# Performance work log

Measured on AMD Instinct MI355X. Metric: run time of the kernel, lower is better.

The kernel has to match this reference:

```python
import jax, jax.numpy as jnp
import numpy as np

B, N, T, L = 32, 716, 168, 64
SED, TED = 32, 4
TN_LAYERS, GCN_LAYERS = 2, 2
TCN_C = 16


def _gru_scan(xseq, Wih, Whh, bih, bhh):
    # torch nn.GRU (batch_first) math; xseq: (B,T,Din) -> (B,T,H)
    Bq = xseq.shape[0]
    H = Whh.shape[1]
    xw = xseq @ Wih.T + bih  # (B,T,3H)

    def step(h, xw_t):
        gh = h @ Whh.T + bhh
        xr, xz, xn = jnp.split(xw_t, 3, axis=-1)
        hr, hz, hn = jnp.split(gh, 3, axis=-1)
        r = jax.nn.sigmoid(xr + hr)
        z = jax.nn.sigmoid(xz + hz)
        n = jnp.tanh(xn + r * hn)
        h_new = (1.0 - z) * n + z * h
        return h_new, h_new

    h0 = jnp.zeros((Bq, H), xseq.dtype)
    _, hs = jax.lax.scan(step, h0, jnp.swapaxes(xw, 0, 1))
    return jnp.swapaxes(hs, 0, 1)


def setup_inputs() -> dict:
    key = jax.random.key(0)
    ks = jax.random.split(key, 20)
    r = lambda k, shp, s: jax.random.normal(k, shp, dtype=jnp.float32) * s
    z = lambda shp: jnp.zeros(shp, jnp.float32)
    din = T + SED
    gin = N + SED + TED
    inp = {
        'x': r(ks[0], (B, N, T), 1.0),
        'x_enc_mark': r(ks[1], (B, T, TED), 1.0),
        'se_emb': r(ks[2], (N, SED), 0.02),
        'se_W1': r(ks[3], (din, L), din ** -0.5), 'se_b1': z((L,)),
        'se_W2': r(ks[4], (L, L), L ** -0.5), 'se_b2': z((L,)),
        'te_emb': r(ks[5], (T, SED), 0.02),
        'te_Wih': r(ks[6], (3 * L, gin), gin ** -0.5),
        'te_Whh': r(ks[7], (3 * L, L), L ** -0.5),
        'te_bih': z((3 * L,)), 'te_bhh': z((3 * L,)),
        'gcn_W': r(ks[8], (TN_LAYERS, GCN_LAYERS, L, L), L ** -0.5),
        'gcn_b': z((TN_LAYERS, GCN_LAYERS, L)),
        'fr_W1': r(ks[9], (L, T), L ** -0.5), 'fr_b1': z((T,)),
        'fr_W2': r(ks[10], (T, T), T ** -0.5), 'fr_b2': z((T,)),
        'tr_Wih': r(ks[11], (3 * N, L), L ** -0.5),
        'tr_Whh': r(ks[12], (3 * N, N), N ** -0.5),
        'tr_bih': z((3 * N,)), 'tr_bhh': z((3 * N,)),
        'tcn_W0': r(ks[13], (TCN_C, 3, 1, 2), (3 * 2) ** -0.5), 'tcn_b0': z((TCN_C,)),
        'tcn_W1': r(ks[14], (TCN_C, TCN_C, 1, 2), (TCN_C * 2) ** -0.5), 'tcn_b1': z((TCN_C,)),
        'tcn_W2': r(ks[15], (TCN_C, TCN_C, 1, 2), (TCN_C * 2) ** -0.5), 'tcn_b2': z((TCN_C,)),
        'out_W': r(ks[16], (1, TCN_C, 1, 1), TCN_C ** -0.5), 'out_b': z((1,)),
    }
    return inp


def reference(x, x_enc_mark, se_emb, se_W1, se_b1, se_W2, se_b2,
              te_emb, te_Wih, te_Whh, te_bih, te_bhh,
              gcn_W, gcn_b, fr_W1, fr_b1, fr_W2, fr_b2,
              tr_Wih, tr_Whh, tr_bih, tr_bhh,
              tcn_W0, tcn_b0, tcn_W1, tcn_b1, tcn_W2, tcn_b2, out_W, out_b):
    Bq, Nq, Tq = x.shape
    elu = jax.nn.elu
    # ---- SpatialEncoder: (B,N,T) -> (B,N,L)
    se_in = jnp.concatenate([x, jnp.broadcast_to(se_emb, (Bq,) + se_emb.shape)], axis=2)
    Xs = elu(se_in @ se_W1 + se_b1) @ se_W2 + se_b2
    # ---- TemporalEncoder: GRU over (B,T,N+SED+TED) -> (B,T,L)
    te_in = jnp.concatenate([jnp.swapaxes(x, 1, 2), x_enc_mark,
                             jnp.broadcast_to(te_emb, (Bq,) + te_emb.shape)], axis=2)
    Xt = _gru_scan(te_in, te_Wih, te_Whh, te_bih, te_bhh)
    X = jnp.concatenate([Xs, Xt], axis=1)  # (B, N+T, L)
    # ---- TN modules: adaptive graph construction + message passing.
    # adj = tanh(relu(X X^T) + I). The torch code extracts nonzero edges per batch
    # and scatters messages over them; since zero weights contribute nothing,
    # edge-list message passing == dense weighted-adjacency matmul (vectorized here).
    eye = jnp.eye(Nq + Tq, dtype=x.dtype)
    for i in range(gcn_W.shape[0]):
        adj = jnp.tanh(jax.nn.relu(jnp.einsum('bnf,bmf->bnm', X, X)) + eye)
        h = X
        for j in range(gcn_W.shape[1]):
            h = elu(jnp.einsum('bnm,bmf->bnf', adj, h) @ gcn_W[i, j] + gcn_b[i, j])
        X = h
    Xs, Xt = X[:, :Nq, :], X[:, Nq:, :]
    # ---- rebuild heads
    n_out = elu(Xs @ fr_W1 + fr_b1) @ fr_W2 + fr_b2  # (B,N,T)
    t_out = _gru_scan(Xt, tr_Wih, tr_Whh, tr_bih, tr_bhh)  # (B,T,N)
    stacked = jnp.stack([n_out, jnp.swapaxes(t_out, 1, 2), x], axis=1)  # (B,3,N,T)
    # ---- TCN output layer: causal dilated convs along time, then 1x1 projection
    dn = ('NCHW', 'OIHW', 'NCHW')
    h = stacked
    for W, b, d in ((tcn_W0, tcn_b0, 1), (tcn_W1, tcn_b1, 2), (tcn_W2, tcn_b2, 4)):
        h = jax.lax.conv_general_dilated(h, W, (1, 1), ((0, 0), (d, 0)),
                                         rhs_dilation=(1, d), dimension_numbers=dn)
        h = elu(h + b[None, :, None, None])
    out = jax.lax.conv_general_dilated(h, out_W, (1, 1), 'VALID',
                                       dimension_numbers=dn) + out_b[None, :, None, None]
    return out[:, :, :, -1]  # (B, 1, N): one-step forecast per node
```

## Files before the change

kernel.cpp:

```cpp
#include <hip/hip_runtime.h>

#define B_   32
#define N_   716
#define T_   168
#define L_   64
#define NT_  884
#define NTP  896
#define TE3_ 192
#define TRH_ 716
#define TR3_ 2148
#define TR3P 2176
#define WSTR 744
#define HSTR 720
#define TRBLKS 90

typedef unsigned short u16;
typedef unsigned long long u64;
typedef __attribute__((ext_vector_type(8))) short short8;
typedef __attribute__((ext_vector_type(4))) float f32x4;

static __device__ __forceinline__ float eluf(float x){ return x > 0.f ? x : expm1f(x); }
static __device__ __forceinline__ float sigf(float x){ return 1.f/(1.f+expf(-x)); }
static __device__ __forceinline__ u16 f2bf(float f){
  unsigned u = __float_as_uint(f);
  unsigned r = (u + 0x7fffu + ((u >> 16) & 1u)) >> 16;
  return (u16)r;
}
static __device__ __forceinline__ float bf2f(u16 h){
  return __uint_as_float(((unsigned)h) << 16);
}
static __device__ __forceinline__ f32x4 bmfma(short8 a, short8 b, f32x4 c){
  return __builtin_amdgcn_mfma_f32_16x16x32_bf16(a, b, c, 0, 0, 0);
}

__global__ __launch_bounds__(256) void k_whhbf(const float* __restrict__ in, u16* __restrict__ out, int n4){
  int i = blockIdx.x*256 + threadIdx.x;
  if (i >= n4) return;
  f32x4 v = *(const f32x4*)(in + (size_t)i*4);
  uint2 p;
  p.x = (unsigned)f2bf(v[0]) | ((unsigned)f2bf(v[1])<<16);
  p.y = (unsigned)f2bf(v[2]) | ((unsigned)f2bf(v[3])<<16);
  *(uint2*)(out + (size_t)i*4) = p;
}
__global__ __launch_bounds__(256) void k_wihbf(const float* __restrict__ Wih, u16* __restrict__ WihB){
  int idx = blockIdx.x*256 + threadIdx.x;
  if (idx >= TR3P*L_) return;
  int r = idx >> 6;
  WihB[idx] = (r < TR3_) ? f2bf(Wih[idx]) : (u16)0;
}
__global__ __launch_bounds__(256) void k_wsmall(
    const float* __restrict__ gW, const float* __restrict__ sW1, const float* __restrict__ sW2,
    const float* __restrict__ fW1, const float* __restrict__ fW2, const float* __restrict__ tW,
    u16* __restrict__ WTh, u16* __restrict__ WTl,
    u16* __restrict__ w1seh, u16* __restrict__ w1sel, u16* __restrict__ w2seh, u16* __restrict__ w2sel,
    u16* __restrict__ w1frh, u16* __restrict__ w1frl, u16* __restrict__ w2frh, u16* __restrict__ w2frl,
    u16* __restrict__ wteB){
  int bid = blockIdx.x, tid = threadIdx.x;
  if (bid < 4){
    int l = bid;
    for (int e = tid; e < 4096; e += 256){
      int g = e >> 6, f = e & 63;
      float v = gW[(size_t)l*4096 + f*64 + g];
      u16 hi = f2bf(v);
      WTh[(size_t)l*4096 + e] = hi;
      WTl[(size_t)l*4096 + e] = f2bf(v - bf2f(hi));
    }
  } else if (bid == 4){
    for (int e = tid; e < 64*224; e += 256){
      int g = e / 224, k = e % 224;
      float v = (k < 200) ? sW1[k*64 + g] : 0.f;
      u16 hi = f2bf(v); w1seh[e] = hi; w1sel[e] = f2bf(v - bf2f(hi));
    }
    for (int e = tid; e < 4096; e += 256){
      int g = e >> 6, f = e & 63;
      float v = sW2[f*64 + g];
      u16 hi = f2bf(v); w2seh[e] = hi; w2sel[e] = f2bf(v - bf2f(hi));
    }
  } else if (bid == 5){
    for (int e = tid; e < 176*64; e += 256){
      int n = e >> 6, k = e & 63;
      float v = (n < 168) ? fW1[k*168 + n] : 0.f;
      u16 hi = f2bf(v); w1frh[e] = hi; w1frl[e] = f2bf(v - bf2f(hi));
    }
    for (int e = tid; e < 16*192; e += 256){
      int c = e / 192, k = e % 192;
      float v = (c < 8 && k < 168) ? fW2[k*168 + 160 + c] : 0.f;
      u16 hi = f2bf(v); w2frh[e] = hi; w2frl[e] = f2bf(v - bf2f(hi));
    }
  } else {
    int idx = (bid - 6)*256 + tid;
    int k = idx % 768;
    float v = (k < 752) ? tW[(size_t)(idx/768)*752 + k] : 0.f;
    wteB[idx] = f2bf(v);
  }
}

__global__ __launch_bounds__(256) void k_sem(const float* __restrict__ x, const float* __restrict__ se_emb,
    const u16* __restrict__ w1h, const u16* __restrict__ w1l,
    const u16* __restrict__ w2h, const u16* __restrict__ w2l,
    const float* __restrict__ b1, const float* __restrict__ b2, float* __restrict__ X){
  __shared__ u16 Sh[64*232], Sl[64*232];
  __shared__ u16 Tlh[64*72], Tll[64*72];
  int m0 = blockIdx.x*64;
  int tid = threadIdx.x, wv = tid >> 6, lane = tid & 63;
  for (int o = tid; o < 64*224; o += 256){
    int r = o / 224, k = o - (o/224)*224;
    int m = m0 + r; int b = m / N_, n = m - b*N_;
    float v = 0.f;
    if (k < 168) v = x[((size_t)b*N_ + n)*T_ + k];
    else if (k < 200) v = se_emb[n*32 + (k - 168)];
    u16 hi = f2bf(v);
    Sh[r*232 + k] = hi; Sl[r*232 + k] = f2bf(v - bf2f(hi));
  }
  __syncthreads();
  const u16* Ah = Sh + (16*wv + (lane & 15))*232 + (lane >> 4)*8;
  const u16* Al = Sl + (16*wv + (lane & 15))*232 + (lane >> 4)*8;
  const u16* Bh = w1h + (lane & 15)*224 + (lane >> 4)*8;
  const u16* Bl = w1l + (lane & 15)*224 + (lane >> 4)*8;
  f32x4 hh[4], hl[4], lh[4];
  #pragma unroll
  for (int q = 0; q < 4; ++q){ hh[q]=(f32x4){0,0,0,0}; hl[q]=(f32x4){0,0,0,0}; lh[q]=(f32x4){0,0,0,0}; }
  #pragma unroll
  for (int kt = 0; kt < 7; ++kt){
    short8 ah = *(const short8*)(Ah + kt*32);
    short8 al = *(const short8*)(Al + kt*32);
    #pragma unroll
    for (int q = 0; q < 4; ++q){
      short8 bh = *(const short8*)(Bh + q*16*224 + kt*32);
      short8 bl = *(const short8*)(Bl + q*16*224 + kt*32);
      hh[q] = bmfma(ah, bh, hh[q]);
      hl[q] = bmfma(ah, bl, hl[q]);
      lh[q] = bmfma(al, bh, lh[q]);
    }
  }
  int mrow = 16*wv + (lane >> 4)*4;
  #pragma unroll
  for (int q = 0; q < 4; ++q){
    int g = q*16 + (lane & 15);
    float bv = b1[g];
    #pragma unroll
    for (int r = 0; r < 4; ++r){
      float v = eluf(hh[q][r] + hl[q][r] + lh[q][r] + bv);
      u16 hi = f2bf(v);
      Tlh[(mrow + r)*72 + g] = hi;
      Tll[(mrow + r)*72 + g] = f2bf(v - bf2f(hi));
    }
  }
  __syncthreads();
  const u16* A2h = Tlh + (16*wv + (lane & 15))*72 + (lane >> 4)*8;
  const u16* A2l = Tll + (16*wv + (lane & 15))*72 + (lane >> 4)*8;
  const u16* B2h = w2h + (lane & 15)*64 + (lane >> 4)*8;
  const u16* B2l = w2l + (lane & 15)*64 + (lane >> 4)*8;
  f32x4 ohh[4], ohl[4], olh[4];
  #pragma unroll
  for (int q = 0; q < 4; ++q){ ohh[q]=(f32x4){0,0,0,0}; ohl[q]=(f32x4){0,0,0,0}; olh[q]=(f32x4){0,0,0,0}; }
  #pragma unroll
  for (int kt = 0; kt < 2; ++kt){
    short8 a2h = *(const short8*)(A2h + kt*32);
    short8 a2l = *(const short8*)(A2l + kt*32);
    #pragma unroll
    for (int q = 0; q < 4; ++q){
      short8 b2h = *(const short8*)(B2h + q*16*64 + kt*32);
      short8 b2l = *(const short8*)(B2l + q*16*64 + kt*32);
      ohh[q] = bmfma(a2h, b2h, ohh[q]);
      ohl[q] = bmfma(a2h, b2l, ohl[q]);
      olh[q] = bmfma(a2l, b2h, olh[q]);
    }
  }
  #pragma unroll
  for (int q = 0; q < 4; ++q){
    int g = q*16 + (lane & 15);
    float bv = b2[g];
    #pragma unroll
    for (int r = 0; r < 4; ++r){
      int m = m0 + mrow + r;
      int b = m / N_, n = m - b*N_;
      X[((size_t)b*NT_ + n)*L_ + g] = ohh[q][r] + ohl[q][r] + olh[q][r] + bv;
    }
  }
}

__global__ __launch_bounds__(256) void k_teinx_b(const float* __restrict__ x, u16* __restrict__ teB){
  __shared__ float tile[32][33];
  int b = blockIdx.z; int n0 = blockIdx.x*32, t0 = blockIdx.y*32;
  int tx = threadIdx.x & 31, ty = threadIdx.x >> 5;
  for (int i = ty; i < 32; i += 8){
    int n = n0 + i, t = t0 + tx;
    if (n < N_ && t < T_) tile[i][tx] = x[((size_t)b*N_ + n)*T_ + t];
  }
  __syncthreads();
  for (int i = ty; i < 32; i += 8){
    int t = t0 + i, n = n0 + tx;
    if (t < T_ && n < N_)
      teB[((size_t)b*T_ + t)*768 + n] = f2bf(tile[tx][i]);
  }
}
__global__ __launch_bounds__(256) void k_teinr_b(const float* __restrict__ mark, const float* __restrict__ te_emb,
                                                 u16* __restrict__ teB){
  int idx = blockIdx.x*256 + threadIdx.x;
  if (idx >= B_*T_*52) return;
  int c = idx % 52; int row = idx / 52; int b = row / T_, t = row % T_;
  float v = 0.f;
  if (c < 4) v = mark[((size_t)b*T_ + t)*4 + c];
  else if (c < 36) v = te_emb[t*32 + (c - 4)];
  teB[(size_t)row*768 + 716 + c] = f2bf(v);
}

__global__ __launch_bounds__(256) void k_texw(const u16* __restrict__ teB, const u16* __restrict__ wteB,
    const float* __restrict__ bih, float* __restrict__ xwte){
  int m0 = blockIdx.x*64, n0 = blockIdx.y*64;
  int tid = threadIdx.x, wv = tid >> 6, lane = tid & 63;
  const u16* Ah = teB + (size_t)(m0 + 16*wv + (lane & 15))*768 + (lane >> 4)*8;
  const u16* Bh = wteB + (size_t)(n0 + (lane & 15))*768 + (lane >> 4)*8;
  f32x4 hh[4];
  #pragma unroll
  for (int q = 0; q < 4; ++q) hh[q]=(f32x4){0,0,0,0};
  #pragma unroll 4
  for (int kt = 0; kt < 24; ++kt){
    short8 ah = *(const short8*)(Ah + kt*32);
    #pragma unroll
    for (int q = 0; q < 4; ++q)
      hh[q] = bmfma(ah, *(const short8*)(Bh + q*16*768 + kt*32), hh[q]);
  }
  int mb = m0 + 16*wv + (lane >> 4)*4;
  #pragma unroll
  for (int q = 0; q < 4; ++q){
    int g = n0 + q*16 + (lane & 15);
    float bv = bih[g];
    #pragma unroll
    for (int r = 0; r < 4; ++r)
      xwte[(size_t)(mb + r)*TE3_ + g] = hh[q][r] + bv;
  }
}

__global__ __launch_bounds__(192) void k_te_scan(const float* __restrict__ xw, const float* __restrict__ Whh,
                 const float* __restrict__ bhh, float* __restrict__ X){
  int b = blockIdx.x; int tid = threadIdx.x;
  __shared__ float Wsh[TE3_*65];
  __shared__ float hs[64];
  __shared__ float gh[TE3_];
  for (int l = tid; l < TE3_*64; l += 192){ int j = l >> 6, f = l & 63; Wsh[j*65+f] = Whh[l]; }
  if (tid < 64) hs[tid] = 0.f;
  __syncthreads();
  for (int t = 0; t < T_; ++t){
    const float* xr = xw + ((size_t)b*T_ + t)*TE3_;
    float g0 = bhh[tid], g1 = 0.f, g2 = 0.f, g3 = 0.f;
    #pragma unroll
    for (int f = 0; f < 64; f += 4){
      g0 = fmaf(hs[f],   Wsh[tid*65+f],   g0);
      g1 = fmaf(hs[f+1], Wsh[tid*65+f+1], g1);
      g2 = fmaf(hs[f+2], Wsh[tid*65+f+2], g2);
      g3 = fmaf(hs[f+3], Wsh[tid*65+f+3], g3);
    }
    gh[tid] = (g0 + g1) + (g2 + g3);
    __syncthreads();
    if (tid < 64){
      float r = sigf(xr[tid] + gh[tid]);
      float z = sigf(xr[64+tid] + gh[64+tid]);
      float n = tanhf(xr[128+tid] + r*gh[128+tid]);
      float hn = (1.f - z)*n + z*hs[tid];
      hs[tid] = hn;
      X[((size_t)b*NT_ + N_ + t)*L_ + tid] = hn;
    }
    __syncthreads();
  }
}

__global__ __launch_bounds__(256) void k_xbf(const float* __restrict__ X,
                 u16* __restrict__ Xbh, u16* __restrict__ Xbl,
                 u16* __restrict__ XTh, u16* __restrict__ XTl){
  __shared__ u16 th[32][33], tl[32][33];
  int b = blockIdx.z, i0 = blockIdx.x*32, f0 = blockIdx.y*32;
  int tx = threadIdx.x & 31, ty = threadIdx.x >> 5;
  for (int rr = ty; rr < 32; rr += 8){
    int i = i0 + rr, f = f0 + tx;
    float v = (i < NT_) ? X[((size_t)b*NT_ + i)*L_ + f] : 0.f;
    u16 hi = f2bf(v);
    u16 lo = f2bf(v - bf2f(hi));
    th[rr][tx] = hi; tl[rr][tx] = lo;
    Xbh[((size_t)b*NTP + i)*L_ + f] = hi;
    Xbl[((size_t)b*NTP + i)*L_ + f] = lo;
  }
  __syncthreads();
  for (int rr = ty; rr < 32; rr += 8){
    XTh[((size_t)b*L_ + f0 + rr)*NTP + i0 + tx] = th[tx][rr];
    XTl[((size_t)b*L_ + f0 + rr)*NTP + i0 + tx] = tl[tx][rr];
  }
}

__global__ __launch_bounds__(256) void k_gcnf(
    const u16* __restrict__ Xbh, const u16* __restrict__ Xbl,
    const u16* __restrict__ hTh, const u16* __restrict__ hTl,
    const u16* __restrict__ WTh, const u16* __restrict__ WTl,
    const float* __restrict__ bias,
    float* __restrict__ Y, u16* __restrict__ YTh, u16* __restrict__ YTl){
  __shared__ u16 AJh[64*72], AJl[64*72];
  __shared__ u16 Tlh[64*72], Tll[64*72];
  int b = blockIdx.y, i0 = blockIdx.x*64;
  int tid = threadIdx.x, wv = tid >> 6, lane = tid & 63;
  const u16* XAh = Xbh + ((size_t)b*NTP + i0 + 16*wv + (lane & 15))*L_ + (lane >> 4)*8;
  const u16* XAl = Xbl + ((size_t)b*NTP + i0 + 16*wv + (lane & 15))*L_ + (lane >> 4)*8;
  const int ib = i0 + 16*wv + (lane >> 4)*4;
  const int mrow = 16*wv + (lane >> 4)*4;
  f32x4 thh[4], thl[4], tlh[4];
  #pragma unroll
  for (int q = 0; q < 4; ++q){ thh[q] = (f32x4){0,0,0,0}; thl[q] = (f32x4){0,0,0,0}; tlh[q] = (f32x4){0,0,0,0}; }
  for (int jt = 0; jt < 14; ++jt){
    int j0 = jt*64;
    {
      const u16* XBh = Xbh + ((size_t)b*NTP + j0 + (lane & 15))*L_ + (lane >> 4)*8;
      const u16* XBl = Xbl + ((size_t)b*NTP + j0 + (lane & 15))*L_ + (lane >> 4)*8;
      f32x4 chh[4], chl[4], clh[4];
      #pragma unroll
      for (int q = 0; q < 4; ++q){ chh[q] = (f32x4){0,0,0,0}; chl[q] = (f32x4){0,0,0,0}; clh[q] = (f32x4){0,0,0,0}; }
      #pragma unroll
      for (int kt = 0; kt < 2; ++kt){
        short8 ah = *(const short8*)(XAh + kt*32);
        short8 al = *(const short8*)(XAl + kt*32);
        #pragma unroll
        for (int q = 0; q < 4; ++q){
          short8 bh = *(const short8*)(XBh + q*16*L_ + kt*32);
          short8 bl = *(const short8*)(XBl + q*16*L_ + kt*32);
          chh[q] = bmfma(ah, bh, chh[q]);
          chl[q] = bmfma(ah, bl, chl[q]);
          clh[q] = bmfma(al, bh, clh[q]);
        }
      }
      int jb = j0 + (lane & 15);
      #pragma unroll
      for (int q = 0; q < 4; ++q){
        int j = jb + q*16;
        #pragma unroll
        for (int r = 0; r < 4; ++r){
          int i = ib + r;
          u16 hi = 0, lo = 0;
          if (i < NT_ && j < NT_){
            float v = tanhf(fmaxf(chh[q][r] + chl[q][r] + clh[q][r], 0.f) + (i == j ? 1.f : 0.f));
            hi = f2bf(v); lo = f2bf(v - bf2f(hi));
          }
          AJh[(mrow + r)*72 + q*16 + (lane & 15)] = hi;
          AJl[(mrow + r)*72 + q*16 + (lane & 15)] = lo;
        }
      }
    }
    __syncthreads();
    {
      const u16* A1h = AJh + (16*wv + (lane & 15))*72 + (lane >> 4)*8;
      const u16* A1l = AJl + (16*wv + (lane & 15))*72 + (lane >> 4)*8;
      const u16* B1h = hTh + ((size_t)b*L_ + (lane & 15))*NTP + j0 + (lane >> 4)*8;
      const u16* B1l = hTl + ((size_t)b*L_ + (lane & 15))*NTP + j0 + (lane >> 4)*8;
      #pragma unroll
      for (int kt = 0; kt < 2; ++kt){
        short8 ah = *(const short8*)(A1h + kt*32);
        short8 al = *(const short8*)(A1l + kt*32);
        #pragma unroll
        for (int q = 0; q < 4; ++q){
          short8 bh = *(const short8*)(B1h + q*16*NTP + kt*32);
          short8 bl = *(const short8*)(B1l + q*16*NTP + kt*32);
          thh[q] = bmfma(ah, bh, thh[q]);
          thl[q] = bmfma(ah, bl, thl[q]);
          tlh[q] = bmfma(al, bh, tlh[q]);
        }
      }
    }
    __syncthreads();
  }
  #pragma unroll
  for (int q = 0; q < 4; ++q)
    #pragma unroll
    for (int r = 0; r < 4; ++r){
      float v = thh[q][r] + thl[q][r] + tlh[q][r];
      u16 hi = f2bf(v);
      Tlh[(mrow + r)*72 + q*16 + (lane & 15)] = hi;
      Tll[(mrow + r)*72 + q*16 + (lane & 15)] = f2bf(v - bf2f(hi));
    }
  __syncthreads();
  const u16* A2h = Tlh + (16*wv + (lane & 15))*72 + (lane >> 4)*8;
  const u16* A2l = Tll + (16*wv + (lane & 15))*72 + (lane >> 4)*8;
  const u16* B2h = WTh + (lane & 15)*L_ + (lane >> 4)*8;
  const u16* B2l = WTl + (lane & 15)*L_ + (lane >> 4)*8;
  f32x4 ohh[4], ohl[4], olh[4];
  #pragma unroll
  for (int q = 0; q < 4; ++q){ ohh[q] = (f32x4){0,0,0,0}; ohl[q] = (f32x4){0,0,0,0}; olh[q] = (f32x4){0,0,0,0}; }
  #pragma unroll
  for (int kt = 0; kt < 2; ++kt){
    short8 a2h = *(const short8*)(A2h + kt*32);
    short8 a2l = *(const short8*)(A2l + kt*32);
    #pragma unroll
    for (int q = 0; q < 4; ++q){
      short8 b2h = *(const short8*)(B2h + q*16*L_ + kt*32);
      short8 b2l = *(const short8*)(B2l + q*16*L_ + kt*32);
      ohh[q] = bmfma(a2h, b2h, ohh[q]);
      ohl[q] = bmfma(a2h, b2l, ohl[q]);
      olh[q] = bmfma(a2l, b2h, olh[q]);
    }
  }
  __syncthreads();
  #pragma unroll
  for (int q = 0; q < 4; ++q){
    int g = q*16 + (lane & 15);
    float bv = bias[g];
    #pragma unroll
    for (int r = 0; r < 4; ++r){
      int i = i0 + mrow + r;
      float v = eluf(ohh[q][r] + ohl[q][r] + olh[q][r] + bv);
      if (i < NT_ && Y) Y[((size_t)b*NT_ + i)*L_ + g] = v;
      u16 hi = 0, lo = 0;
      if (i < NT_){ hi = f2bf(v); lo = f2bf(v - bf2f(hi)); }
      Tlh[g*72 + mrow + r] = hi;
      Tll[g*72 + mrow + r] = lo;
    }
  }
  __syncthreads();
  {
    int g = tid >> 2, c = tid & 3;
    uint4* dh = (uint4*)(YTh + ((size_t)b*L_ + g)*NTP + i0 + c*16);
    uint4* dl = (uint4*)(YTl + ((size_t)b*L_ + g)*NTP + i0 + c*16);
    const uint4* sh = (const uint4*)(Tlh + g*72 + c*16);
    const uint4* sl = (const uint4*)(Tll + g*72 + c*16);
    dh[0] = sh[0]; dh[1] = sh[1];
    dl[0] = sl[0]; dl[1] = sl[1];
  }
}

__global__ __launch_bounds__(256) void k_frm(const float* __restrict__ X,
    const u16* __restrict__ w1h, const u16* __restrict__ w1l,
    const u16* __restrict__ w2h, const u16* __restrict__ w2l,
    const float* __restrict__ b1, const float* __restrict__ b2, float* __restrict__ nout8){
  __shared__ u16 Sh[64*72], Sl[64*72];
  __shared__ u16 T1h[64*192], T1l[64*192];
  __shared__ u16 B2hl[16*192], B2ll[16*192];
  int m0 = blockIdx.x*64;
  int tid = threadIdx.x, wv = tid >> 6, lane = tid & 63;
  for (int o = tid; o < 768; o += 256){
    ((u64*)B2hl)[o] = ((const u64*)w2h)[o];
    ((u64*)B2ll)[o] = ((const u64*)w2l)[o];
  }
  for (int o = tid; o < 1024; o += 256){
    int rr = o >> 4, cc = o & 15;
    T1h[rr*192 + 176 + cc] = 0; T1l[rr*192 + 176 + cc] = 0;
  }
  for (int o = tid; o < 4096; o += 256){
    int r = o >> 6, k = o & 63;
    int m = m0 + r; int ab = m / N_, an = m - ab*N_;
    float v = X[((size_t)ab*NT_ + an)*L_ + k];
    u16 hi = f2bf(v);
    Sh[r*72 + k] = hi; Sl[r*72 + k] = f2bf(v - bf2f(hi));
  }
  __syncthreads();
  const u16* Ah = Sh + (16*wv + (lane & 15))*72 + (lane >> 4)*8;
  const u16* Al = Sl + (16*wv + (lane & 15))*72 + (lane >> 4)*8;
  int mrow = 16*wv + (lane >> 4)*4;
  for (int tile = 0; tile < 11; ++tile){
    const u16* Bh = w1h + (tile*16 + (lane & 15))*64 + (lane >> 4)*8;
    const u16* Bl = w1l + (tile*16 + (lane & 15))*64 + (lane >> 4)*8;
    f32x4 shh={0,0,0,0}, shl={0,0,0,0}, slh={0,0,0,0};
    #pragma unroll
    for (int kt = 0; kt < 2; ++kt){
      short8 ah = *(const short8*)(Ah + kt*32);
      short8 al = *(const short8*)(Al + kt*32);
      short8 bh = *(const short8*)(Bh + kt*32);
      short8 bl = *(const short8*)(Bl + kt*32);
      shh = bmfma(ah, bh, shh);
      shl = bmfma(ah, bl, shl);
      slh = bmfma(al, bh, slh);
    }
    int col = tile*16 + (lane & 15);
    float bb = (col < 168) ? b1[col] : 0.f;
    #pragma unroll
    for (int r = 0; r < 4; ++r){
      float v = (col < 168) ? eluf(shh[r] + shl[r] + slh[r] + bb) : 0.f;
      u16 hi = f2bf(v);
      T1h[(mrow + r)*192 + col] = hi;
      T1l[(mrow + r)*192 + col] = f2bf(v - bf2f(hi));
    }
  }
  __syncthreads();
  const u16* A2h = T1h + (16*wv + (lane & 15))*192 + (lane >> 4)*8;
  const u16* A2l = T1l + (16*wv + (lane & 15))*192 + (lane >> 4)*8;
  const u16* Bh2 = B2hl + (lane & 15)*192 + (lane >> 4)*8;
  const u16* Bl2 = B2ll + (lane & 15)*192 + (lane >> 4)*8;
  f32x4 ohh={0,0,0,0}, ohl={0,0,0,0}, olh={0,0,0,0};
  #pragma unroll
  for (int kt = 0; kt < 6; ++kt){
    short8 a2h = *(const short8*)(A2h + kt*32);
    short8 a2l = *(const short8*)(A2l + kt*32);
    short8 b2h = *(const short8*)(Bh2 + kt*32);
    short8 b2l = *(const short8*)(Bl2 + kt*32);
    ohh = bmfma(a2h, b2h, ohh);
    ohl = bmfma(a2h, b2l, ohl);
    olh = bmfma(a2l, b2h, olh);
  }
  int c = lane & 15;
  if (c < 8){
    float bv = b2[160 + c];
    #pragma unroll
    for (int r = 0; r < 4; ++r){
      int m = m0 + mrow + r;
      nout8[(size_t)m*8 + c] = ohh[r] + ohl[r] + olh[r] + bv;
    }
  }
}

__global__ __launch_bounds__(256) void k_xwm2(const float* __restrict__ X, const u16* __restrict__ WihB,
                                              const float* __restrict__ bih, u16* __restrict__ xwB){
  int m0 = blockIdx.x*64, n0 = blockIdx.y*64;
  int tid = threadIdx.x, wv = tid >> 6, lane = tid & 63;
  int am = m0 + 16*wv + (lane & 15);
  int t = am >> 5, b = am & 31;
  const float* Arow = X + ((size_t)b*NT_ + N_ + t)*L_ + (lane >> 4)*8;
  const u16* Bb = WihB + (size_t)(n0 + (lane & 15))*L_ + (lane >> 4)*8;
  f32x4 c0={0,0,0,0}, c1={0,0,0,0}, c2={0,0,0,0}, c3={0,0,0,0};
  #pragma unroll
  for (int kt = 0; kt < 2; ++kt){
    f32x4 f0 = *(const f32x4*)(Arow + kt*32);
    f32x4 f1 = *(const f32x4*)(Arow + kt*32 + 4);
    short8 a;
    a[0]=(short)f2bf(f0[0]); a[1]=(short)f2bf(f0[1]); a[2]=(short)f2bf(f0[2]); a[3]=(short)f2bf(f0[3]);
    a[4]=(short)f2bf(f1[0]); a[5]=(short)f2bf(f1[1]); a[6]=(short)f2bf(f1[2]); a[7]=(short)f2bf(f1[3]);
    c0 = bmfma(a, *(const short8*)(Bb + kt*32), c0);
    c1 = bmfma(a, *(const short8*)(Bb + 16*L_ + kt*32), c1);
    c2 = bmfma(a, *(const short8*)(Bb + 32*L_ + kt*32), c2);
    c3 = bmfma(a, *(const short8*)(Bb + 48*L_ + kt*32), c3);
  }
  int mb = m0 + 16*wv + (lane >> 4)*4;
  int nb = n0 + (lane & 15);
  f32x4 cc[4] = {c0, c1, c2, c3};
  #pragma unroll
  for (int q = 0; q < 4; ++q){
    int n = nb + q*16;
    if (n >= TR3_) continue;
    float bv = bih[n];
    #pragma unroll
    for (int r = 0; r < 4; ++r)
      xwB[(size_t)(mb + r)*TR3_ + n] = f2bf(cc[q][r] + bv);
  }
}

__global__ __launch_bounds__(192) void k_tr_scan(
    const u16* __restrict__ WhhB,
    const float* __restrict__ bhh,
    const u16* __restrict__ xwB,
    u16* __restrict__ hb0, u16* __restrict__ hb1,
    float* __restrict__ tout8,
    int* __restrict__ flags){
  __shared__ u16 w_lds[48*WSTR];
  __shared__ u16 h_lds[16*WSTR];
  __shared__ float g_lds[2*256];
  __shared__ u64 xw_ldsq[2][192];
  const int tid = threadIdx.x;
  const int wv = tid >> 6, lane = tid & 63;
  const int cb = blockIdx.x >> 1, hhalf = blockIdx.x & 1;
  const int k0 = cb*16, b0 = hhalf*16;
  const int prow = tid / 12, pc = tid % 12;
  const int pg = pc >> 2, pko = (pc & 3)*4;

  xw_ldsq[0][prow*12 + pc] =
    *(const u64*)(xwB + (size_t)(b0 + prow)*TR3_ + pg*TRH_ + k0 + pko);
  for (int o = tid; o < 16*24; o += 192){
    int n = o / 24, c = o - n*24;
    h_lds[n*WSTR + 720 + c] = 0;
  }
  for (int r = 0; r < 48; ++r){
    int g = r >> 4, m = r & 15, k = k0 + m;
    bool kv = (k < TRH_);
    const uint2* src = (const uint2*)(WhhB + (size_t)(g*TRH_ + (kv ? k : 0))*TRH_);
    uint2* dst = (uint2*)(w_lds + r*WSTR);
    uint2 zz; zz.x = 0; zz.y = 0;
    for (int o = tid; o < 186; o += 192)
      dst[o] = (kv && o < 179) ? src[o] : zz;
  }
  const u16* arow = w_lds + (size_t)(wv*16 + (lane & 15))*WSTR + (lane >> 4)*8;
  const u16* brow = h_lds + (size_t)(lane & 15)*WSTR + (lane >> 4)*8;

  const int mb = (lane >> 4)*4;
  const int kx = k0 + mb;
  const bool kval = (kx < TRH_);
  const int bx = b0 + (lane & 15);
  f32x4 hp = {0.f, 0.f, 0.f, 0.f};
  f32x4 br4 = {0,0,0,0}, bz4 = {0,0,0,0}, bn4 = {0,0,0,0};
  if (wv == 0){
    int kc = kval ? kx : 0;
    br4 = *(const f32x4*)(bhh + kc);
    bz4 = *(const f32x4*)(bhh + TRH_ + kc);
    bn4 = *(const f32x4*)(bhh + 2*TRH_ + kc);
  }
  const int sn = tid / 12, sj = tid % 12;
  __syncthreads();

  for (int t = 0; t < T_; ++t){
    const u16* hcur = (t & 1) ? hb1 : hb0;
    u16* hnxt = (t & 1) ? hb0 : hb1;
    {
      const u64* srow = (const u64*)(hcur + (size_t)(b0 + sn)*HSTR) + sj;
      u64 v0  = __hip_atomic_load(srow +   0, __ATOMIC_RELAXED, __HIP_MEMORY_SCOPE_AGENT);
      u64 v1  = __hip_atomic_load(srow +  12, __ATOMIC_RELAXED, __HIP_MEMORY_SCOPE_AGENT);
      u64 v2  = __hip_atomic_load(srow +  24, __ATOMIC_RELAXED, __HIP_MEMORY_SCOPE_AGENT);
      u64 v3  = __hip_atomic_load(srow +  36, __ATOMIC_RELAXED, __HIP_MEMORY_SCOPE_AGENT);
      u64 v4  = __hip_atomic_load(srow +  48, __ATOMIC_RELAXED, __HIP_MEMORY_SCOPE_AGENT);
      u64 v5  = __hip_atomic_load(srow +  60, __ATOMIC_RELAXED, __HIP_MEMORY_SCOPE_AGENT);
      u64 v6  = __hip_atomic_load(srow +  72, __ATOMIC_RELAXED, __HIP_MEMORY_SCOPE_AGENT);
      u64 v7  = __hip_atomic_load(srow +  84, __ATOMIC_RELAXED, __HIP_MEMORY_SCOPE_AGENT);
      u64 v8  = __hip_atomic_load(srow +  96, __ATOMIC_RELAXED, __HIP_MEMORY_SCOPE_AGENT);
      u64 v9  = __hip_atomic_load(srow + 108, __ATOMIC_RELAXED, __HIP_MEMORY_SCOPE_AGENT);
      u64 v10 = __hip_atomic_load(srow + 120, __ATOMIC_RELAXED, __HIP_MEMORY_SCOPE_AGENT);
      u64 v11 = __hip_atomic_load(srow + 132, __ATOMIC_RELAXED, __HIP_MEMORY_SCOPE_AGENT);
      u64 v12 = __hip_atomic_load(srow + 144, __ATOMIC_RELAXED, __HIP_MEMORY_SCOPE_AGENT);
      u64 v13 = __hip_atomic_load(srow + 156, __ATOMIC_RELAXED, __HIP_MEMORY_SCOPE_AGENT);
      u64 v14 = __hip_atomic_load(srow + 168, __ATOMIC_RELAXED, __HIP_MEMORY_SCOPE_AGENT);
      u64* d = (u64*)(h_lds + sn*WSTR) + sj;
      d[0]   = v0;   d[12]  = v1;   d[24]  = v2;   d[36]  = v3;
      d[48]  = v4;   d[60]  = v5;   d[72]  = v6;   d[84]  = v7;
      d[96]  = v8;   d[108] = v9;   d[120] = v10;  d[132] = v11;
      d[144] = v12;  d[156] = v13;  d[168] = v14;
    }
    __syncthreads();
    u64 pf = 0;
    const bool haspf = (t + 1 < T_);
    if (haspf)
      pf = *(const u64*)(xwB + (size_t)((t+1)*32 + b0 + prow)*TR3_ + pg*TRH_ + k0 + pko);
    f32x4 a0={0,0,0,0}, a1={0,0,0,0}, a2={0,0,0,0}, a3={0,0,0,0};
    for (int kt = 0; kt < 20; kt += 4){
      a0 = bmfma(*(const short8*)(arow + kt*32),     *(const short8*)(brow + kt*32),     a0);
      a1 = bmfma(*(const short8*)(arow + (kt+1)*32), *(const short8*)(brow + (kt+1)*32), a1);
      a2 = bmfma(*(const short8*)(arow + (kt+2)*32), *(const short8*)(brow + (kt+2)*32), a2);
      a3 = bmfma(*(const short8*)(arow + (kt+3)*32), *(const short8*)(brow + (kt+3)*32), a3);
    }
    a0 = bmfma(*(const short8*)(arow + 20*32), *(const short8*)(brow + 20*32), a0);
    a1 = bmfma(*(const short8*)(arow + 21*32), *(const short8*)(brow + 21*32), a1);
    a2 = bmfma(*(const short8*)(arow + 22*32), *(const short8*)(brow + 22*32), a2);
    f32x4 acc = (a0 + a1) + (a2 + a3);
    if (wv){
      #pragma unroll
      for (int r = 0; r < 4; ++r) g_lds[(wv-1)*256 + lane*4 + r] = acc[r];
    }
    __syncthreads();
    if (wv == 0){
      if (kval){
        const u16* xb = ((const u16*)&xw_ldsq[t & 1][0]) + (lane & 15)*48;
        float hnew[4];
        #pragma unroll
        for (int r = 0; r < 4; ++r){
          float rg = sigf(bf2f(xb[mb + r]) + acc[r] + br4[r]);
          float zg = sigf(bf2f(xb[16 + mb + r]) + g_lds[lane*4 + r] + bz4[r]);
          float ng = tanhf(bf2f(xb[32 + mb + r]) + rg*(g_lds[256 + lane*4 + r] + bn4[r]));
          hnew[r] = (1.f - zg)*ng + zg*hp[r];
          hp[r] = hnew[r];
        }
        u64 pk = (u64)((unsigned)f2bf(hnew[0]) | ((unsigned)f2bf(hnew[1]) << 16))
               | ((u64)((unsigned)f2bf(hnew[2]) | ((unsigned)f2bf(hnew[3]) << 16)) << 32);
        __hip_atomic_store((u64*)(hnxt + (size_t)bx*HSTR + kx), pk,
                           __ATOMIC_RELAXED, __HIP_MEMORY_SCOPE_AGENT);
        if (t >= 160){
          #pragma unroll
          for (int r = 0; r < 4; ++r)
            tout8[(size_t)(bx*TRH_ + kx + r)*8 + (t - 160)] = hnew[r];
        }
      }
      asm volatile("s_waitcnt vmcnt(0)" ::: "memory");
      if (lane == 0)
        __hip_atomic_store(flags + blockIdx.x*16, t + 1,
                           __ATOMIC_RELAXED, __HIP_MEMORY_SCOPE_AGENT);
    }
    if (wv == 1 && lane < 45 && t + 1 < T_){
      const int* fp = flags + (lane*2 + hhalf)*16;
      while (__hip_atomic_load(fp, __ATOMIC_RELAXED, __HIP_MEMORY_SCOPE_AGENT) < t + 1){}
    }
    if (haspf) xw_ldsq[(t + 1) & 1][prow*12 + pc] = pf;
    __syncthreads();
  }
}

__global__ __launch_bounds__(256) void k_tcn(const float* __restrict__ nout8, const float* __restrict__ tout8,
                 const float* __restrict__ x,
                 const float* __restrict__ W0, const float* __restrict__ b0,
                 const float* __restrict__ W1, const float* __restrict__ b1,
                 const float* __restrict__ W2, const float* __restrict__ b2,
                 const float* __restrict__ oW, const float* __restrict__ ob,
                 float* __restrict__ out){
  __shared__ float w0s[96], b0s[16], w1s[512], b1s[16], w2s[512], b2s[16], ows[16], obs;
  int tid = threadIdx.x;
  for (int l = tid; l < 96; l += 256) w0s[l] = W0[l];
  for (int l = tid; l < 512; l += 256){ w1s[l] = W1[l]; w2s[l] = W2[l]; }
  if (tid < 16){ b0s[tid]=b0[tid]; b1s[tid]=b1[tid]; b2s[tid]=b2[tid]; ows[tid]=oW[tid]; }
  if (tid == 0) obs = ob[0];
  __syncthreads();
  int idx = blockIdx.x*256 + tid;
  if (idx >= B_*N_) return;
  int b = idx / N_, n = idx % N_;
  float s0[8], s1[8], s2[8];
  #pragma unroll
  for (int i = 0; i < 8; ++i){
    s0[i] = nout8[(size_t)idx*8 + i];
    s1[i] = tout8[(size_t)idx*8 + i];
    s2[i] = x[((size_t)b*N_ + n)*T_ + 160 + i];
  }
  float h1[16][4];
  #pragma unroll
  for (int c = 0; c < 16; ++c)
    #pragma unroll
    for (int q = 0; q < 4; ++q){
      int tt = 2*q + 1;
      float v = b0s[c]
        + w0s[c*6+0]*s0[tt-1] + w0s[c*6+1]*s0[tt]
        + w0s[c*6+2]*s1[tt-1] + w0s[c*6+3]*s1[tt]
        + w0s[c*6+4]*s2[tt-1] + w0s[c*6+5]*s2[tt];
      h1[c][q] = eluf(v);
    }
  float h2[16][2];
  #pragma unroll
  for (int c = 0; c < 16; ++c){
    float v3 = b1s[c], v7 = b1s[c];
    #pragma unroll
    for (int i2 = 0; i2 < 16; ++i2){
      v3 += w1s[c*32+i2*2]*h1[i2][0] + w1s[c*32+i2*2+1]*h1[i2][1];
      v7 += w1s[c*32+i2*2]*h1[i2][2] + w1s[c*32+i2*2+1]*h1[i2][3];
    }
    h2[c][0] = eluf(v3); h2[c][1] = eluf(v7);
  }
  float o = obs;
  #pragma unroll
  for (int c = 0; c < 16; ++c){
    float v = b2s[c];
    #pragma unroll
    for (int i2 = 0; i2 < 16; ++i2)
      v += w2s[c*32+i2*2]*h2[i2][0] + w2s[c*32+i2*2+1]*h2[i2][1];
    o += ows[c]*eluf(v);
  }
  out[idx] = o;
}

extern "C" void kernel_launch(void* const* d_in, const int* in_sizes, int n_in,
                              void* d_out, int out_size, void* d_ws, size_t ws_size,
                              hipStream_t stream){
  const float* x       = (const float*)d_in[0];
  const float* mark    = (const float*)d_in[1];
  const float* se_emb  = (const float*)d_in[2];
  const float* se_W1   = (const float*)d_in[3];
  const float* se_b1   = (const float*)d_in[4];
  const float* se_W2   = (const float*)d_in[5];
  const float* se_b2   = (const float*)d_in[6];
  const float* te_emb  = (const float*)d_in[7];
  const float* te_Wih  = (const float*)d_in[8];
  const float* te_Whh  = (const float*)d_in[9];
  const float* te_bih  = (const float*)d_in[10];
  const float* te_bhh  = (const float*)d_in[11];
  const float* gcn_W   = (const float*)d_in[12];
  const float* gcn_b   = (const float*)d_in[13];
  const float* fr_W1   = (const float*)d_in[14];
  const float* fr_b1   = (const float*)d_in[15];
  const float* fr_W2   = (const float*)d_in[16];
  const float* fr_b2   = (const float*)d_in[17];
  const float* tr_Wih  = (const float*)d_in[18];
  const float* tr_Whh  = (const float*)d_in[19];
  const float* tr_bih  = (const float*)d_in[20];
  const float* tr_bhh  = (const float*)d_in[21];
  const float* tcn_W0  = (const float*)d_in[22];
  const float* tcn_b0  = (const float*)d_in[23];
  const float* tcn_W1  = (const float*)d_in[24];
  const float* tcn_b1  = (const float*)d_in[25];
  const float* tcn_W2  = (const float*)d_in[26];
  const float* tcn_b2  = (const float*)d_in[27];
  const float* out_W   = (const float*)d_in[28];
  const float* out_b   = (const float*)d_in[29];
  float* out = (float*)d_out;
  (void)in_sizes; (void)n_in; (void)out_size; (void)ws_size;

  char* ws = (char*)d_ws;
  size_t off = 0;
  auto alloc = [&](size_t bytes)->void*{
    void* p = (void*)(ws + off); off += (bytes + 255) & ~(size_t)255; return p; };
  float* X       = (float*)alloc((size_t)B_*NT_*L_*4);
  u16*   teinB   = (u16*)  alloc((size_t)B_*T_*768*2);
  float* te_xw   = (float*)alloc((size_t)B_*T_*TE3_*4);
  u16*   xwB     = (u16*)  alloc((size_t)B_*T_*TR3_*2);
  u16*   WihB    = (u16*)  alloc((size_t)TR3P*L_*2);
  u16*   WhhB    = (u16*)  alloc((size_t)TR3_*TRH_*2);
  u16*   Xbh     = (u16*)  alloc((size_t)B_*NTP*L_*2);
  u16*   Xbl     = (u16*)  alloc((size_t)B_*NTP*L_*2);
  u16*   hTah    = (u16*)  alloc((size_t)B_*L_*NTP*2);
  u16*   hTal    = (u16*)  alloc((size_t)B_*L_*NTP*2);
  u16*   hTbh    = (u16*)  alloc((size_t)B_*L_*NTP*2);
  u16*   hTbl    = (u16*)  alloc((size_t)B_*L_*NTP*2);
  u16*   WTh     = (u16*)  alloc((size_t)4*4096*2);
  u16*   WTl     = (u16*)  alloc((size_t)4*4096*2);
  u16*   w1seh   = (u16*)  alloc((size_t)64*224*2);
  u16*   w1sel   = (u16*)  alloc((size_t)64*224*2);
  u16*   w2seh   = (u16*)  alloc((size_t)4096*2);
  u16*   w2sel   = (u16*)  alloc((size_t)4096*2);
  u16*   w1frh   = (u16*)  alloc((size_t)176*64*2);
  u16*   w1frl   = (u16*)  alloc((size_t)176*64*2);
  u16*   w2frh   = (u16*)  alloc((size_t)16*192*2);
  u16*   w2frl   = (u16*)  alloc((size_t)16*192*2);
  u16*   wteB    = (u16*)  alloc((size_t)192*768*2);
  u16*   hb0     = (u16*)  alloc((size_t)B_*HSTR*2);
  u16*   hb1     = (u16*)  alloc((size_t)B_*HSTR*2);
  int*   flags   = (int*)  alloc(8192);
  float* nout8   = (float*)alloc((size_t)B_*N_*8*4);
  float* tout8   = (float*)alloc((size_t)B_*N_*8*4);

  hipMemsetAsync(hb0, 0, (size_t)B_*HSTR*2*2 + 8192, stream);

  k_whhbf<<<(TR3_*TRH_/4 + 255)/256, 256, 0, stream>>>(tr_Whh, WhhB, TR3_*TRH_/4);
  k_wihbf<<<(TR3P*L_ + 255)/256, 256, 0, stream>>>(tr_Wih, WihB);
  k_wsmall<<<582, 256, 0, stream>>>(gcn_W, se_W1, se_W2, fr_W1, fr_W2, te_Wih,
      WTh, WTl, w1seh, w1sel, w2seh, w2sel, w1frh, w1frl, w2frh, w2frl, wteB);
  k_sem<<<358, 256, 0, stream>>>(x, se_emb, w1seh, w1sel, w2seh, w2sel, se_b1, se_b2, X);
  k_teinx_b<<<dim3(23,6,B_), 256, 0, stream>>>(x, teinB);
  k_teinr_b<<<(B_*T_*52 + 255)/256, 256, 0, stream>>>(mark, te_emb, teinB);
  k_texw<<<dim3(84,3), 256, 0, stream>>>(teinB, wteB, te_bih, te_xw);
  k_te_scan<<<B_, 192, 0, stream>>>(te_xw, te_Whh, te_bhh, X);
  for (int i = 0; i < 2; ++i){
    k_xbf<<<dim3(28,2,B_),256,0,stream>>>(X, Xbh, Xbl, hTah, hTal);
    k_gcnf<<<dim3(14,B_),256,0,stream>>>(Xbh, Xbl, hTah, hTal,
        WTh + (i*2+0)*4096, WTl + (i*2+0)*4096, gcn_b + (i*2+0)*64, nullptr, hTbh, hTbl);
    k_gcnf<<<dim3(14,B_),256,0,stream>>>(Xbh, Xbl, hTbh, hTbl,
        WTh + (i*2+1)*4096, WTl + (i*2+1)*4096, gcn_b + (i*2+1)*64, X, hTah, hTal);
  }
  k_frm<<<358, 256, 0, stream>>>(X, w1frh, w1frl, w2frh, w2frl, fr_b1, fr_b2, nout8);
  k_xwm2<<<dim3(84,34),256,0,stream>>>(X, WihB, tr_bih, xwB);
  k_tr_scan<<<TRBLKS,192,0,stream>>>(WhhB, tr_bhh, xwB, hb0, hb1, tout8, flags);
  k_tcn<<<(B_*N_+255)/256,256,0,stream>>>(nout8, tout8, x,
      tcn_W0, tcn_b0, tcn_W1, tcn_b1, tcn_W2, tcn_b2, out_W, out_b, out);
}
```

Measured before the change: 1.435 ms.

## Merge prep and back-end kernels and move scan flag wait to step start

Three weight-conversion kernels become one k_prep launch, and the frm and xw projection kernels become one k_back launch that picks its work by block index. This cuts launch overhead and lets independent work run concurrently. In the GRU scan, the cross-block flag spin-wait moves from the end of each step to the start and is followed by a barrier. All 45 lanes of a 192-thread block now wait, where before only wave 1 did, and the trailing barrier is gone. The new sync ordering needs care: the xw prefetch store into LDS now has no barrier after it before the next iteration's wait.

```diff
diff --git a/kernel.cpp b/kernel.cpp
--- a/kernel.cpp
+++ b/kernel.cpp
@@ -33,22 +33,9 @@
   return __builtin_amdgcn_mfma_f32_16x16x32_bf16(a, b, c, 0, 0, 0);
 }
 
-__global__ __launch_bounds__(256) void k_whhbf(const float* __restrict__ in, u16* __restrict__ out, int n4){
-  int i = blockIdx.x*256 + threadIdx.x;
-  if (i >= n4) return;
-  f32x4 v = *(const f32x4*)(in + (size_t)i*4);
-  uint2 p;
-  p.x = (unsigned)f2bf(v[0]) | ((unsigned)f2bf(v[1])<<16);
-  p.y = (unsigned)f2bf(v[2]) | ((unsigned)f2bf(v[3])<<16);
-  *(uint2*)(out + (size_t)i*4) = p;
-}
-__global__ __launch_bounds__(256) void k_wihbf(const float* __restrict__ Wih, u16* __restrict__ WihB){
-  int idx = blockIdx.x*256 + threadIdx.x;
-  if (idx >= TR3P*L_) return;
-  int r = idx >> 6;
-  WihB[idx] = (r < TR3_) ? f2bf(Wih[idx]) : (u16)0;
-}
-__global__ __launch_bounds__(256) void k_wsmall(
+__global__ __launch_bounds__(256) void k_prep(
+    const float* __restrict__ whh, u16* __restrict__ WhhB,
+    const float* __restrict__ wih, u16* __restrict__ WihB,
     const float* __restrict__ gW, const float* __restrict__ sW1, const float* __restrict__ sW2,
     const float* __restrict__ fW1, const float* __restrict__ fW2, const float* __restrict__ tW,
     u16* __restrict__ WTh, u16* __restrict__ WTl,
@@ -56,8 +43,21 @@
     u16* __restrict__ w1frh, u16* __restrict__ w1frl, u16* __restrict__ w2frh, u16* __restrict__ w2frl,
     u16* __restrict__ wteB){
   int bid = blockIdx.x, tid = threadIdx.x;
-  if (bid < 4){
-    int l = bid;
+  if (bid < 1502){
+    int i = bid*256 + tid;
+    if (i < TR3_*TRH_/4){
+      f32x4 v = *(const f32x4*)(whh + (size_t)i*4);
+      uint2 p;
+      p.x = (unsigned)f2bf(v[0]) | ((unsigned)f2bf(v[1])<<16);
+      p.y = (unsigned)f2bf(v[2]) | ((unsigned)f2bf(v[3])<<16);
+      *(uint2*)(WhhB + (size_t)i*4) = p;
+    }
+  } else if (bid < 2046){
+    int idx = (bid - 1502)*256 + tid;
+    int r = idx >> 6;
+    WihB[idx] = (r < TR3_) ? f2bf(wih[idx]) : (u16)0;
+  } else if (bid < 2050){
+    int l = bid - 2046;
     for (int e = tid; e < 4096; e += 256){
       int g = e >> 6, f = e & 63;
       float v = gW[(size_t)l*4096 + f*64 + g];
@@ -65,7 +65,7 @@
       WTh[(size_t)l*4096 + e] = hi;
       WTl[(size_t)l*4096 + e] = f2bf(v - bf2f(hi));
     }
-  } else if (bid == 4){
+  } else if (bid == 2050){
     for (int e = tid; e < 64*224; e += 256){
       int g = e / 224, k = e % 224;
       float v = (k < 200) ? sW1[k*64 + g] : 0.f;
@@ -76,7 +76,7 @@
       float v = sW2[f*64 + g];
       u16 hi = f2bf(v); w2seh[e] = hi; w2sel[e] = f2bf(v - bf2f(hi));
     }
-  } else if (bid == 5){
+  } else if (bid == 2051){
     for (int e = tid; e < 176*64; e += 256){
       int n = e >> 6, k = e & 63;
       float v = (n < 168) ? fW1[k*168 + n] : 0.f;
@@ -88,7 +88,7 @@
       u16 hi = f2bf(v); w2frh[e] = hi; w2frl[e] = f2bf(v - bf2f(hi));
     }
   } else {
-    int idx = (bid - 6)*256 + tid;
+    int idx = (bid - 2052)*256 + tid;
     int k = idx % 768;
     float v = (k < 752) ? tW[(size_t)(idx/768)*752 + k] : 0.f;
     wteB[idx] = f2bf(v);
@@ -423,15 +423,50 @@
   }
 }
 
-__global__ __launch_bounds__(256) void k_frm(const float* __restrict__ X,
+__global__ __launch_bounds__(256) void k_back(const float* __restrict__ X,
     const u16* __restrict__ w1h, const u16* __restrict__ w1l,
     const u16* __restrict__ w2h, const u16* __restrict__ w2l,
-    const float* __restrict__ b1, const float* __restrict__ b2, float* __restrict__ nout8){
+    const float* __restrict__ b1, const float* __restrict__ b2, float* __restrict__ nout8,
+    const u16* __restrict__ WihB, const float* __restrict__ bih, u16* __restrict__ xwB){
   __shared__ u16 Sh[64*72], Sl[64*72];
   __shared__ u16 T1h[64*192], T1l[64*192];
   __shared__ u16 B2hl[16*192], B2ll[16*192];
+  int tid = threadIdx.x, wv = tid >> 6, lane = tid & 63;
+  if (blockIdx.x >= 358){
+    int r = blockIdx.x - 358;
+    int m0 = (r % 84)*64, n0 = (r / 84)*64;
+    int am = m0 + 16*wv + (lane & 15);
+    int t = am >> 5, b = am & 31;
+    const float* Arow = X + ((size_t)b*NT_ + N_ + t)*L_ + (lane >> 4)*8;
+    const u16* Bb = WihB + (size_t)(n0 + (lane & 15))*L_ + (lane >> 4)*8;
+    f32x4 c0={0,0,0,0}, c1={0,0,0,0}, c2={0,0,0,0}, c3={0,0,0,0};
+    #pragma unroll
+    for (int kt = 0; kt < 2; ++kt){
+      f32x4 f0 = *(const f32x4*)(Arow + kt*32);
+      f32x4 f1 = *(const f32x4*)(Arow + kt*32 + 4);
+      short8 a;
+      a[0]=(short)f2bf(f0[0]); a[1]=(short)f2bf(f0[1]); a[2]=(short)f2bf(f0[2]); a[3]=(short)f2bf(f0[3]);
+      a[4]=(short)f2bf(f1[0]); a[5]=(short)f2bf(f1[1]); a[6]=(short)f2bf(f1[2]); a[7]=(short)f2bf(f1[3]);
+      c0 = bmfma(a, *(const short8*)(Bb + kt*32), c0);
+      c1 = bmfma(a, *(const short8*)(Bb + 16*L_ + kt*32), c1);
+      c2 = bmfma(a, *(const short8*)(Bb + 32*L_ + kt*32), c2);
+      c3 = bmfma(a, *(const short8*)(Bb + 48*L_ + kt*32), c3);
+    }
+    int mb = m0 + 16*wv + (lane >> 4)*4;
+    int nb = n0 + (lane & 15);
+    f32x4 cc[4] = {c0, c1, c2, c3};
+    #pragma unroll
+    for (int q = 0; q < 4; ++q){
+      int n = nb + q*16;
+      if (n >= TR3_) continue;
+      float bv = bih[n];
+      #pragma unroll
+      for (int rr = 0; rr < 4; ++rr)
+        xwB[(size_t)(mb + rr)*TR3_ + n] = f2bf(cc[q][rr] + bv);
+    }
+    return;
+  }
   int m0 = blockIdx.x*64;
-  int tid = threadIdx.x, wv = tid >> 6, lane = tid & 63;
   for (int o = tid; o < 768; o += 256){
     ((u64*)B2hl)[o] = ((const u64*)w2h)[o];
     ((u64*)B2ll)[o] = ((const u64*)w2l)[o];
@@ -499,41 +534,6 @@
       int m = m0 + mrow + r;
       nout8[(size_t)m*8 + c] = ohh[r] + ohl[r] + olh[r] + bv;
     }
-  }
-}
-
-__global__ __launch_bounds__(256) void k_xwm2(const float* __restrict__ X, const u16* __restrict__ WihB,
-                                              const float* __restrict__ bih, u16* __restrict__ xwB){
-  int m0 = blockIdx.x*64, n0 = blockIdx.y*64;
-  int tid = threadIdx.x, wv = tid >> 6, lane = tid & 63;
-  int am = m0 + 16*wv + (lane & 15);
-  int t = am >> 5, b = am & 31;
-  const float* Arow = X + ((size_t)b*NT_ + N_ + t)*L_ + (lane >> 4)*8;
-  const u16* Bb = WihB + (size_t)(n0 + (lane & 15))*L_ + (lane >> 4)*8;
-  f32x4 c0={0,0,0,0}, c1={0,0,0,0}, c2={0,0,0,0}, c3={0,0,0,0};
-  #pragma unroll
-  for (int kt = 0; kt < 2; ++kt){
-    f32x4 f0 = *(const f32x4*)(Arow + kt*32);
-    f32x4 f1 = *(const f32x4*)(Arow + kt*32 + 4);
-    short8 a;
-    a[0]=(short)f2bf(f0[0]); a[1]=(short)f2bf(f0[1]); a[2]=(short)f2bf(f0[2]); a[3]=(short)f2bf(f0[3]);
-    a[4]=(short)f2bf(f1[0]); a[5]=(short)f2bf(f1[1]); a[6]=(short)f2bf(f1[2]); a[7]=(short)f2bf(f1[3]);
-    c0 = bmfma(a, *(const short8*)(Bb + kt*32), c0);
-    c1 = bmfma(a, *(const short8*)(Bb + 16*L_ + kt*32), c1);
-    c2 = bmfma(a, *(const short8*)(Bb + 32*L_ + kt*32), c2);
-    c3 = bmfma(a, *(const short8*)(Bb + 48*L_ + kt*32), c3);
-  }
-  int mb = m0 + 16*wv + (lane >> 4)*4;
-  int nb = n0 + (lane & 15);
-  f32x4 cc[4] = {c0, c1, c2, c3};
-  #pragma unroll
-  for (int q = 0; q < 4; ++q){
-    int n = nb + q*16;
-    if (n >= TR3_) continue;
-    float bv = bih[n];
-    #pragma unroll
-    for (int r = 0; r < 4; ++r)
-      xwB[(size_t)(mb + r)*TR3_ + n] = f2bf(cc[q][r] + bv);
   }
 }
 
@@ -591,6 +591,11 @@
   for (int t = 0; t < T_; ++t){
     const u16* hcur = (t & 1) ? hb1 : hb0;
     u16* hnxt = (t & 1) ? hb0 : hb1;
+    if (tid < 45){
+      const int* fp = flags + (tid*2 + hhalf)*16;
+      while (__hip_atomic_load(fp, __ATOMIC_RELAXED, __HIP_MEMORY_SCOPE_AGENT) < t){}
+    }
+    __syncthreads();
     {
       const u64* srow = (const u64*)(hcur + (size_t)(b0 + sn)*HSTR) + sj;
       u64 v0  = __hip_atomic_load(srow +   0, __ATOMIC_RELAXED, __HIP_MEMORY_SCOPE_AGENT);
@@ -662,12 +667,7 @@
         __hip_atomic_store(flags + blockIdx.x*16, t + 1,
                            __ATOMIC_RELAXED, __HIP_MEMORY_SCOPE_AGENT);
     }
-    if (wv == 1 && lane < 45 && t + 1 < T_){
-      const int* fp = flags + (lane*2 + hhalf)*16;
-      while (__hip_atomic_load(fp, __ATOMIC_RELAXED, __HIP_MEMORY_SCOPE_AGENT) < t + 1){}
-    }
     if (haspf) xw_ldsq[(t + 1) & 1][prow*12 + pc] = pf;
-    __syncthreads();
   }
 }
 
@@ -801,9 +801,8 @@
 
   hipMemsetAsync(hb0, 0, (size_t)B_*HSTR*2*2 + 8192, stream);
 
-  k_whhbf<<<(TR3_*TRH_/4 + 255)/256, 256, 0, stream>>>(tr_Whh, WhhB, TR3_*TRH_/4);
-  k_wihbf<<<(TR3P*L_ + 255)/256, 256, 0, stream>>>(tr_Wih, WihB);
-  k_wsmall<<<582, 256, 0, stream>>>(gcn_W, se_W1, se_W2, fr_W1, fr_W2, te_Wih,
+  k_prep<<<2628, 256, 0, stream>>>(tr_Whh, WhhB, tr_Wih, WihB,
+      gcn_W, se_W1, se_W2, fr_W1, fr_W2, te_Wih,
       WTh, WTl, w1seh, w1sel, w2seh, w2sel, w1frh, w1frl, w2frh, w2frl, wteB);
   k_sem<<<358, 256, 0, stream>>>(x, se_emb, w1seh, w1sel, w2seh, w2sel, se_b1, se_b2, X);
   k_teinx_b<<<dim3(23,6,B_), 256, 0, stream>>>(x, teinB);
@@ -817,8 +816,8 @@
     k_gcnf<<<dim3(14,B_),256,0,stream>>>(Xbh, Xbl, hTbh, hTbl,
         WTh + (i*2+1)*4096, WTl + (i*2+1)*4096, gcn_b + (i*2+1)*64, X, hTah, hTal);
   }
-  k_frm<<<358, 256, 0, stream>>>(X, w1frh, w1frl, w2frh, w2frl, fr_b1, fr_b2, nout8);
-  k_xwm2<<<dim3(84,34),256,0,stream>>>(X, WihB, tr_bih, xwB);
+  k_back<<<358 + 84*34, 256, 0, stream>>>(X, w1frh, w1frl, w2frh, w2frl, fr_b1, fr_b2, nout8,
+      WihB, tr_bih, xwB);
   k_tr_scan<<<TRBLKS,192,0,stream>>>(WhhB, tr_bhh, xwB, hb0, hb1, tout8, flags);
   k_tcn<<<(B_*N_+255)/256,256,0,stream>>>(nout8, tout8, x,
       tcn_W0, tcn_b0, tcn_W1, tcn_b1, tcn_W2, tcn_b2, out_W, out_b, out);
```

New measurement: 1.419 ms. No clear change (-1.1%).
